# Optimization experiments

Hardware: AMD Instinct MI355X
Metric: run time of the kernel (lower is better)

Reference implementation:

```python
import jax, jax.numpy as jnp
import numpy as np

# --- fixed OpenCV filter kernels ---
# cv2.getGaussianKernel(3, 1): exp(-(i-1)^2/2), normalized -> [0.27407, 0.45186, 0.27407]
_g = np.exp(-((np.arange(3) - 1.0) ** 2) / 2.0)
GAUSS_1D = (_g / _g.sum()).astype(np.float32)
# cv2 Sobel/Laplacian ksize=9 separable parts (unnormalized, as cv2.Laplacian uses):
#   smoothing = binomial row C(8,k); second derivative = C(6,k) conv [1,-2,1]
SMOOTH_9 = np.array([1, 8, 28, 56, 70, 56, 28, 8, 1], dtype=np.float32)
D2_9 = np.array([1, 4, 4, -4, -10, -4, 4, 4, 1], dtype=np.float32)


def _depthwise_conv(x, k2d):
    """Depthwise 2D correlation with BORDER_REFLECT_101 padding (cv2 default).

    x: [N,H,W,C] float, k2d: [kh,kw] float (symmetric, so corr == conv)."""
    C = x.shape[-1]
    rh, rw = k2d.shape[0] // 2, k2d.shape[1] // 2
    # jnp 'reflect' == OpenCV BORDER_REFLECT_101 (edge pixel not duplicated)
    xp = jnp.pad(x, ((0, 0), (rh, rh), (rw, rw), (0, 0)), mode='reflect')
    k = jnp.broadcast_to(k2d[:, :, None, None], (k2d.shape[0], k2d.shape[1], 1, C))
    return jax.lax.conv_general_dilated(
        xp, k, window_strides=(1, 1), padding='VALID',
        dimension_numbers=('NHWC', 'HWIO', 'NHWC'),
        feature_group_count=C)


def setup_inputs() -> dict:
    key = jax.random.key(0)
    # uint8-range image batch, as the original layer feeds uint8 data to OpenCV
    x = jax.random.uniform(key, (32, 512, 512, 3), dtype=jnp.float32) * 255.0
    return {"x": x}


def reference(x) -> jnp.ndarray:
    g = jnp.asarray(GAUSS_1D)
    blur = _depthwise_conv(x, jnp.outer(g, g))  # GaussianBlur(ksize=3, sigma=1)
    lap_k = jnp.asarray(np.outer(SMOOTH_9, D2_9) + np.outer(D2_9, SMOOTH_9))
    lap = _depthwise_conv(blur, lap_k) + 1.0  # delta = 1
    # CV_8UC1 destination depth -> saturate to [0, 255]
    return jnp.clip(lap, 0.0, 255.0)
```

## Files before the change

### kernel.cpp

```cpp
#include <hip/hip_runtime.h>


#define TH 16
#define TW 32
#define FW (TW*3)
#define BF ((TW+8)*3)
#define BH (TH+8)
#define PH (TH+2)
#define VW 124
#define PW 108
#define HIMG 512
#define WIMG 512
#define ROWF (WIMG*3)

#define OFF_B 3120
#define SM_TOTAL 6000

__device__ __forceinline__ int reflect101(int i, int n) {
    i = (i < 0) ? -i : i;
    return (i >= n) ? (2 * n - 2 - i) : i;
}

__device__ __forceinline__ float c6dot(float f0, float f1, float f2, float f3,
                                       float f4, float f5, float f6) {
    return fmaf(20.f, f3, fmaf(6.f, f1 + f5, fmaf(15.f, f2 + f4, f0 + f6)));
}

__device__ __forceinline__ float4 c6dot4(const float4& a, const float4& b, const float4& c,
                                         const float4& d, const float4& e, const float4& f,
                                         const float4& g) {
    return make_float4(c6dot(a.x, b.x, c.x, d.x, e.x, f.x, g.x),
                       c6dot(a.y, b.y, c.y, d.y, e.y, f.y, g.y),
                       c6dot(a.z, b.z, c.z, d.z, e.z, f.z, g.z),
                       c6dot(a.w, b.w, c.w, d.w, e.w, f.w, g.w));
}

__device__ __forceinline__ float4 g3(const float4& a, const float4& b, const float4& c,
                                     float G0, float G1) {
    return make_float4(G0 * (a.x + c.x) + G1 * b.x,
                       G0 * (a.y + c.y) + G1 * b.y,
                       G0 * (a.z + c.z) + G1 * b.z,
                       G0 * (a.w + c.w) + G1 * b.w);
}

__global__ __launch_bounds__(256, 6)
void log_fused(const float* __restrict__ x, float* __restrict__ out) {
    __shared__ __align__(16) float smem[SM_TOTAL];
    float* const hblur = smem;
    float* const vq    = smem;
    float* const blur  = smem + OFF_B;
    float* const P     = smem + OFF_B;

    const int tid  = threadIdx.x;
    const int col0 = blockIdx.x * TW;
    const int row0 = blockIdx.y * TH;
    const int n    = blockIdx.z;

    const int R0    = max(0, row0 - 5);
    const int R1    = min(HIMG - 1, row0 + TH + 4);
    const int nrows = R1 - R0 + 1;

    const float G0 = 0.2740686190f, G1 = 0.4518627620f;

    const bool edgecol = (col0 == 0) || (col0 + TW == WIMG);
    if (!edgecol) {
        if (tid < 240) {
            const int cg = tid % 30;
            const int rg = tid / 30;
            const float* xb = x + ((size_t)n * HIMG + (size_t)(R0 + rg)) * ROWF
                                + (3 * (col0 - 4) + 4 * cg - 4);
            float* hb = hblur + rg * BF + 4 * cg;
            for (int r = rg; r < nrows; r += 8, xb += 8 * ROWF, hb += 8 * BF) {
                const float4 a = *(const float4*)(xb);
                const float4 b = *(const float4*)(xb + 4);
                const float4 c = *(const float4*)(xb + 8);
                float4 o;
                o.x = G0 * (a.y + b.w) + G1 * b.x;
                o.y = G0 * (a.z + c.x) + G1 * b.y;
                o.z = G0 * (a.w + c.y) + G1 * b.z;
                o.w = G0 * (b.x + c.z) + G1 * b.w;
                *(float4*)hb = o;
            }
        }
    } else {
        if (tid < 240) {
            const int lc  = tid % BF;
            const int rg  = tid / BF;
            const int lcp = lc / 3;
            const int ch  = lc - 3 * lcp;
            const int gc  = reflect101(col0 - 4 + lcp, WIMG);
            const int xm  = reflect101(gc - 1, WIMG) * 3 + ch;
            const int x0  = gc * 3 + ch;
            const int xp  = reflect101(gc + 1, WIMG) * 3 + ch;
            const float* xr = x + ((size_t)n * HIMG + (size_t)(R0 + rg)) * ROWF;
            for (int r = rg; r < nrows; r += 2, xr += 2 * ROWF) {
                hblur[r * BF + lc] = G0 * (xr[xm] + xr[xp]) + G1 * xr[x0];
            }
        }
    }
    __syncthreads();

    if (row0 > 0 && row0 + TH < HIMG) {
        for (int g = tid; g < 12 * 30; g += 256) {
            const int lp = g / 30;
            const int qc = g - lp * 30;
            const float* hb = hblur + (2 * lp) * BF + qc * 4;
            const float4 w0 = *(const float4*)(hb);
            const float4 w1 = *(const float4*)(hb + BF);
            const float4 w2 = *(const float4*)(hb + 2 * BF);
            const float4 w3 = *(const float4*)(hb + 3 * BF);
            float* bp = blur + (2 * lp) * BF + qc * 4;
            *(float4*)bp        = g3(w0, w1, w2, G0, G1);
            *(float4*)(bp + BF) = g3(w1, w2, w3, G0, G1);
        }
    } else {
        for (int g = tid; g < 12 * 30; g += 256) {
            const int lp = g / 30;
            const int qc = g - lp * 30;
            const int gg = row0 - 4 + 2 * lp;
            const int y0 = reflect101(gg, HIMG);
            const int y1 = reflect101(gg + 1, HIMG);
            const int lc = qc * 4;
            const float4 a0 = *(const float4*)&hblur[(reflect101(y0 - 1, HIMG) - R0) * BF + lc];
            const float4 a1 = *(const float4*)&hblur[(y0 - R0) * BF + lc];
            const float4 a2 = *(const float4*)&hblur[(reflect101(y0 + 1, HIMG) - R0) * BF + lc];
            const float4 b0 = *(const float4*)&hblur[(reflect101(y1 - 1, HIMG) - R0) * BF + lc];
            const float4 b1 = *(const float4*)&hblur[(y1 - R0) * BF + lc];
            const float4 b2 = *(const float4*)&hblur[(reflect101(y1 + 1, HIMG) - R0) * BF + lc];
            float* bp = blur + (2 * lp) * BF + lc;
            *(float4*)bp        = g3(a0, a1, a2, G0, G1);
            *(float4*)(bp + BF) = g3(b0, b1, b2, G0, G1);
        }
    }
    __syncthreads();

    for (int g = tid; g < 9 * 30; g += 256) {
        const int lp = g / 30;
        const int qc = g - lp * 30;
        const float* bp = blur + (2 * lp) * BF + qc * 4;
        float4 w[8];
        #pragma unroll
        for (int k = 0; k < 8; ++k)
            w[k] = *(const float4*)(bp + k * BF);
        float* vp = vq + (2 * lp) * VW + qc * 4;
        *(float4*)vp        = c6dot4(w[0], w[1], w[2], w[3], w[4], w[5], w[6]);
        *(float4*)(vp + VW) = c6dot4(w[1], w[2], w[3], w[4], w[5], w[6], w[7]);
    }
    __syncthreads();

    for (int g = tid; g < PH * 13; g += 256) {
        const int r  = g / 13;
        const int qp = g - r * 13;
        const float* v = vq + r * VW + qp * 8;
        float f[28];
        #pragma unroll
        for (int q = 0; q < 7; ++q) {
            const float4 w = *(const float4*)(v + 4 * q);
            f[4*q+0] = w.x; f[4*q+1] = w.y; f[4*q+2] = w.z; f[4*q+3] = w.w;
        }
        float p[8];
        #pragma unroll
        for (int j = 0; j < 8; ++j)
            p[j] = c6dot(f[j], f[j+3], f[j+6], f[j+9], f[j+12], f[j+15], f[j+18]);
        float* pr = P + r * PW + qp * 8;
        *(float4*)pr       = make_float4(p[0], p[1], p[2], p[3]);
        *(float4*)(pr + 4) = make_float4(p[4], p[5], p[6], p[7]);
    }
    __syncthreads();

    float* const outn = out + (size_t)n * HIMG * ROWF;
    for (int g = tid; g < TH * 12; g += 256) {
        const int i  = g / 12;
        const int qp = g - i * 12;
        const int o  = qp * 8;
        const float* pt = P + i * PW + o;
        const float* pm = pt + PW;
        const float* pb = pm + PW;
        float t[16], m[16], b[16];
        #pragma unroll
        for (int q = 0; q < 4; ++q) {
            const float4 vt = *(const float4*)(pt + 4 * q);
            t[4*q+0] = vt.x; t[4*q+1] = vt.y; t[4*q+2] = vt.z; t[4*q+3] = vt.w;
            const float4 vm = *(const float4*)(pm + 4 * q);
            m[4*q+0] = vm.x; m[4*q+1] = vm.y; m[4*q+2] = vm.z; m[4*q+3] = vm.w;
            const float4 vb = *(const float4*)(pb + 4 * q);
            b[4*q+0] = vb.x; b[4*q+1] = vb.y; b[4*q+2] = vb.z; b[4*q+3] = vb.w;
        }
        float o8[8];
        #pragma unroll
        for (int j = 0; j < 8; ++j) {
            const float c = m[j + 3];
            const float s = (t[j] - c) + (t[j + 6] - c) + (b[j] - c) + (b[j + 6] - c);
            const float v = fmaf(2.f, s, 1.f);
            o8[j] = fminf(fmaxf(v, 0.f), 255.f);
        }
        float* op = outn + (size_t)(row0 + i) * ROWF + (size_t)(col0 * 3 + o);
        *(float4*)op       = make_float4(o8[0], o8[1], o8[2], o8[3]);
        *(float4*)(op + 4) = make_float4(o8[4], o8[5], o8[6], o8[7]);
    }
}

extern "C" void kernel_launch(void* const* d_in, const int* in_sizes, int n_in,
                              void* d_out, int out_size, void* d_ws, size_t ws_size,
                              hipStream_t stream) {
    const float* x = (const float*)d_in[0];
    float* outp = (float*)d_out;
    const int nimg = in_sizes[0] / (HIMG * WIMG * 3);
    dim3 grid(WIMG / TW, HIMG / TH, nimg);
    log_fused<<<grid, dim3(256, 1, 1), 0, stream>>>(x, outp);
}
```

Before: 223.1 us.

## Fold Gaussian blur into binomial filter taps for interior tiles

For interior tiles, the 3-tap Gaussian is folded into the 7-tap binomial smoothing by convolving them analytically into a 9-tap kernel (U0..U4). Vertical and horizontal passes then read global memory directly and skip the separate blur stages and two barriers. Edge tiles now compute the 2D blur straight from global memory with reflect indexing in one pass, which lets shared memory shrink so launch bounds can rise to 8 blocks per SM. The cost is more global loads per thread (ten rows of float4) and different rounding from the folded coefficients.

New measurement: 327.0 us. +46.5%, slower.

```diff
diff --git a/kernel.cpp b/kernel.cpp
--- a/kernel.cpp
+++ b/kernel.cpp
@@ -3,22 +3,27 @@
 
 #define TH 16
 #define TW 32
-#define FW (TW*3)
-#define BF ((TW+8)*3)
-#define BH (TH+8)
-#define PH (TH+2)
-#define VW 124
-#define PW 108
 #define HIMG 512
 #define WIMG 512
 #define ROWF (WIMG*3)
 
-#define OFF_B 3120
-#define SM_TOTAL 6000
+#define VUW 132
+#define PW  108
+#define BLW 120
+#define VQW 124
+
+#define OFF_P  2376
+#define OFF_BL 2232
+#define SM_TOTAL 5112
 
 __device__ __forceinline__ int reflect101(int i, int n) {
     i = (i < 0) ? -i : i;
     return (i >= n) ? (2 * n - 2 - i) : i;
+}
+
+__device__ __forceinline__ float4 fma4(float s, const float4& a, const float4& b) {
+    return make_float4(fmaf(s, a.x, b.x), fmaf(s, a.y, b.y),
+                       fmaf(s, a.z, b.z), fmaf(s, a.w, b.w));
 }
 
 __device__ __forceinline__ float c6dot(float f0, float f1, float f2, float f3,
@@ -43,130 +48,165 @@
                        G0 * (a.w + c.w) + G1 * b.w);
 }
 
-__global__ __launch_bounds__(256, 6)
+#define U0 0.27406862f
+#define U1 2.09627447f
+#define U2 7.09627447f
+#define U3 13.90372553f
+#define U4 17.25931382f
+
+__global__ __launch_bounds__(256, 8)
 void log_fused(const float* __restrict__ x, float* __restrict__ out) {
     __shared__ __align__(16) float smem[SM_TOTAL];
-    float* const hblur = smem;
-    float* const vq    = smem;
-    float* const blur  = smem + OFF_B;
-    float* const P     = smem + OFF_B;
+    float* const vU   = smem;
+    float* const vq   = smem;
+    float* const blur = smem + OFF_BL;
+    float* const P    = smem + OFF_P;
 
     const int tid  = threadIdx.x;
     const int col0 = blockIdx.x * TW;
     const int row0 = blockIdx.y * TH;
     const int n    = blockIdx.z;
-
-    const int R0    = max(0, row0 - 5);
-    const int R1    = min(HIMG - 1, row0 + TH + 4);
-    const int nrows = R1 - R0 + 1;
+    const float* const xi = x + (size_t)n * HIMG * ROWF;
 
     const float G0 = 0.2740686190f, G1 = 0.4518627620f;
 
-    const bool edgecol = (col0 == 0) || (col0 + TW == WIMG);
-    if (!edgecol) {
-        if (tid < 240) {
-            const int cg = tid % 30;
-            const int rg = tid / 30;
-            const float* xb = x + ((size_t)n * HIMG + (size_t)(R0 + rg)) * ROWF
-                                + (3 * (col0 - 4) + 4 * cg - 4);
-            float* hb = hblur + rg * BF + 4 * cg;
-            for (int r = rg; r < nrows; r += 8, xb += 8 * ROWF, hb += 8 * BF) {
-                const float4 a = *(const float4*)(xb);
-                const float4 b = *(const float4*)(xb + 4);
-                const float4 c = *(const float4*)(xb + 8);
-                float4 o;
-                o.x = G0 * (a.y + b.w) + G1 * b.x;
-                o.y = G0 * (a.z + c.x) + G1 * b.y;
-                o.z = G0 * (a.w + c.y) + G1 * b.z;
-                o.w = G0 * (b.x + c.z) + G1 * b.w;
-                *(float4*)hb = o;
-            }
-        }
+    const bool interior = (row0 != 0) && (row0 != HIMG - TH) &&
+                          (col0 != 0) && (col0 != WIMG - TW);
+
+    if (interior) {
+        const float Uk[10] = {U0, U1, U2, U3, U4, U3, U2, U1, U0, 0.f};
+        for (int g = tid; g < 288; g += 256) {
+            const int q  = g & 31;
+            const int rp = g >> 5;
+            const float* xp = xi + (size_t)(row0 - 5 + 2 * rp) * ROWF
+                                 + (3 * col0 - 16 + 4 * q);
+            float4 a0 = make_float4(0.f, 0.f, 0.f, 0.f), a1 = a0;
+            #pragma unroll
+            for (int j = 0; j < 10; ++j) {
+                const float4 w = *(const float4*)(xp + (size_t)j * ROWF);
+                if (j < 9) a0 = fma4(Uk[j], w, a0);
+                if (j > 0) a1 = fma4(Uk[j - 1], w, a1);
+            }
+            float* vp = vU + (2 * rp) * VUW + 4 * q;
+            *(float4*)vp         = a0;
+            *(float4*)(vp + VUW) = a1;
+        }
+        __syncthreads();
+
+        if (tid < 234) {
+            const int t = tid % 13;
+            const int v = tid / 13;
+            const float* vr = vU + v * VUW + 8 * t;
+            float f[36];
+            #pragma unroll
+            for (int c = 0; c < 9; ++c) {
+                const float4 w = *(const float4*)(vr + 4 * c);
+                f[4*c+0] = w.x; f[4*c+1] = w.y; f[4*c+2] = w.z; f[4*c+3] = w.w;
+            }
+            float p[8];
+            #pragma unroll
+            for (int j = 0; j < 8; ++j) {
+                const float t0 = f[j + 1]  + f[j + 25];
+                const float t1 = f[j + 4]  + f[j + 22];
+                const float t2 = f[j + 7]  + f[j + 19];
+                const float t3 = f[j + 10] + f[j + 16];
+                p[j] = fmaf(U0, t0, fmaf(U1, t1, fmaf(U2, t2,
+                           fmaf(U3, t3, U4 * f[j + 13]))));
+            }
+            float* pr = P + v * PW + 8 * t;
+            *(float4*)pr       = make_float4(p[0], p[1], p[2], p[3]);
+            *(float4*)(pr + 4) = make_float4(p[4], p[5], p[6], p[7]);
+        }
+        __syncthreads();
     } else {
-        if (tid < 240) {
-            const int lc  = tid % BF;
-            const int rg  = tid / BF;
-            const int lcp = lc / 3;
-            const int ch  = lc - 3 * lcp;
-            const int gc  = reflect101(col0 - 4 + lcp, WIMG);
-            const int xm  = reflect101(gc - 1, WIMG) * 3 + ch;
-            const int x0  = gc * 3 + ch;
-            const int xp  = reflect101(gc + 1, WIMG) * 3 + ch;
-            const float* xr = x + ((size_t)n * HIMG + (size_t)(R0 + rg)) * ROWF;
-            for (int r = rg; r < nrows; r += 2, xr += 2 * ROWF) {
-                hblur[r * BF + lc] = G0 * (xr[xm] + xr[xp]) + G1 * xr[x0];
-            }
-        }
-    }
-    __syncthreads();
-
-    if (row0 > 0 && row0 + TH < HIMG) {
-        for (int g = tid; g < 12 * 30; g += 256) {
+        for (int e = tid; e < 720; e += 256) {
+            const int br = e / 30;
+            const int qc = e - br * 30;
+            const int gg = row0 - 4 + br;
+            const int gr = reflect101(gg, HIMG);
+            const int ym = reflect101(gr - 1, HIMG);
+            const int yp = reflect101(gr + 1, HIMG);
+            const int lcpmin = (4 * qc) / 3;
+            const int lcpmax = (4 * qc + 3) / 3;
+            const bool safe = (col0 - 5 + lcpmin >= 0) && (col0 - 3 + lcpmax <= WIMG - 1);
+            float4 r;
+            if (safe) {
+                const int fb = 3 * col0 - 16 + 4 * qc;
+                const float* r0 = xi + (size_t)ym * ROWF + fb;
+                const float* r1 = xi + (size_t)gr * ROWF + fb;
+                const float* r2 = xi + (size_t)yp * ROWF + fb;
+                float4 h[3];
+                #pragma unroll
+                for (int rr = 0; rr < 3; ++rr) {
+                    const float* rp = (rr == 0) ? r0 : (rr == 1) ? r1 : r2;
+                    const float4 a = *(const float4*)(rp);
+                    const float4 b = *(const float4*)(rp + 4);
+                    const float4 c = *(const float4*)(rp + 8);
+                    h[rr] = make_float4(G0 * (a.y + b.w) + G1 * b.x,
+                                        G0 * (a.z + c.x) + G1 * b.y,
+                                        G0 * (a.w + c.y) + G1 * b.z,
+                                        G0 * (b.x + c.z) + G1 * b.w);
+                }
+                r = g3(h[0], h[1], h[2], G0, G1);
+            } else {
+                float o[4];
+                #pragma unroll
+                for (int m = 0; m < 4; ++m) {
+                    const int lc  = 4 * qc + m;
+                    const int lcp = lc / 3;
+                    const int ch  = lc - 3 * lcp;
+                    const int gc  = reflect101(col0 - 4 + lcp, WIMG);
+                    const int xm  = reflect101(gc - 1, WIMG) * 3 + ch;
+                    const int x0  = gc * 3 + ch;
+                    const int xp2 = reflect101(gc + 1, WIMG) * 3 + ch;
+                    const float* r0 = xi + (size_t)ym * ROWF;
+                    const float* r1 = xi + (size_t)gr * ROWF;
+                    const float* r2 = xi + (size_t)yp * ROWF;
+                    const float h0 = G0 * (r0[xm] + r0[xp2]) + G1 * r0[x0];
+                    const float h1 = G0 * (r1[xm] + r1[xp2]) + G1 * r1[x0];
+                    const float h2 = G0 * (r2[xm] + r2[xp2]) + G1 * r2[x0];
+                    o[m] = G0 * (h0 + h2) + G1 * h1;
+                }
+                r = make_float4(o[0], o[1], o[2], o[3]);
+            }
+            *(float4*)&blur[br * BLW + 4 * qc] = r;
+        }
+        __syncthreads();
+
+        for (int g = tid; g < 270; g += 256) {
             const int lp = g / 30;
             const int qc = g - lp * 30;
-            const float* hb = hblur + (2 * lp) * BF + qc * 4;
-            const float4 w0 = *(const float4*)(hb);
-            const float4 w1 = *(const float4*)(hb + BF);
-            const float4 w2 = *(const float4*)(hb + 2 * BF);
-            const float4 w3 = *(const float4*)(hb + 3 * BF);
-            float* bp = blur + (2 * lp) * BF + qc * 4;
-            *(float4*)bp        = g3(w0, w1, w2, G0, G1);
-            *(float4*)(bp + BF) = g3(w1, w2, w3, G0, G1);
-        }
-    } else {
-        for (int g = tid; g < 12 * 30; g += 256) {
-            const int lp = g / 30;
-            const int qc = g - lp * 30;
-            const int gg = row0 - 4 + 2 * lp;
-            const int y0 = reflect101(gg, HIMG);
-            const int y1 = reflect101(gg + 1, HIMG);
-            const int lc = qc * 4;
-            const float4 a0 = *(const float4*)&hblur[(reflect101(y0 - 1, HIMG) - R0) * BF + lc];
-            const float4 a1 = *(const float4*)&hblur[(y0 - R0) * BF + lc];
-            const float4 a2 = *(const float4*)&hblur[(reflect101(y0 + 1, HIMG) - R0) * BF + lc];
-            const float4 b0 = *(const float4*)&hblur[(reflect101(y1 - 1, HIMG) - R0) * BF + lc];
-            const float4 b1 = *(const float4*)&hblur[(y1 - R0) * BF + lc];
-            const float4 b2 = *(const float4*)&hblur[(reflect101(y1 + 1, HIMG) - R0) * BF + lc];
-            float* bp = blur + (2 * lp) * BF + lc;
-            *(float4*)bp        = g3(a0, a1, a2, G0, G1);
-            *(float4*)(bp + BF) = g3(b0, b1, b2, G0, G1);
-        }
+            const float* bp = blur + (2 * lp) * BLW + 4 * qc;
+            float4 w[8];
+            #pragma unroll
+            for (int k = 0; k < 8; ++k)
+                w[k] = *(const float4*)(bp + k * BLW);
+            float* vp = vq + (2 * lp) * VQW + 4 * qc;
+            *(float4*)vp         = c6dot4(w[0], w[1], w[2], w[3], w[4], w[5], w[6]);
+            *(float4*)(vp + VQW) = c6dot4(w[1], w[2], w[3], w[4], w[5], w[6], w[7]);
+        }
+        __syncthreads();
+
+        if (tid < 234) {
+            const int t = tid % 13;
+            const int r = tid / 13;
+            const float* v = vq + r * VQW + 8 * t;
+            float f[28];
+            #pragma unroll
+            for (int c = 0; c < 7; ++c) {
+                const float4 w = *(const float4*)(v + 4 * c);
+                f[4*c+0] = w.x; f[4*c+1] = w.y; f[4*c+2] = w.z; f[4*c+3] = w.w;
+            }
+            float p[8];
+            #pragma unroll
+            for (int j = 0; j < 8; ++j)
+                p[j] = c6dot(f[j], f[j+3], f[j+6], f[j+9], f[j+12], f[j+15], f[j+18]);
+            float* pr = P + r * PW + 8 * t;
+            *(float4*)pr       = make_float4(p[0], p[1], p[2], p[3]);
+            *(float4*)(pr + 4) = make_float4(p[4], p[5], p[6], p[7]);
+        }
+        __syncthreads();
     }
-    __syncthreads();
-
-    for (int g = tid; g < 9 * 30; g += 256) {
-        const int lp = g / 30;
-        const int qc = g - lp * 30;
-        const float* bp = blur + (2 * lp) * BF + qc * 4;
-        float4 w[8];
-        #pragma unroll
-        for (int k = 0; k < 8; ++k)
-            w[k] = *(const float4*)(bp + k * BF);
-        float* vp = vq + (2 * lp) * VW + qc * 4;
-        *(float4*)vp        = c6dot4(w[0], w[1], w[2], w[3], w[4], w[5], w[6]);
-        *(float4*)(vp + VW) = c6dot4(w[1], w[2], w[3], w[4], w[5], w[6], w[7]);
-    }
-    __syncthreads();
-
-    for (int g = tid; g < PH * 13; g += 256) {
-        const int r  = g / 13;
-        const int qp = g - r * 13;
-        const float* v = vq + r * VW + qp * 8;
-        float f[28];
-        #pragma unroll
-        for (int q = 0; q < 7; ++q) {
-            const float4 w = *(const float4*)(v + 4 * q);
-            f[4*q+0] = w.x; f[4*q+1] = w.y; f[4*q+2] = w.z; f[4*q+3] = w.w;
-        }
-        float p[8];
-        #pragma unroll
-        for (int j = 0; j < 8; ++j)
-            p[j] = c6dot(f[j], f[j+3], f[j+6], f[j+9], f[j+12], f[j+15], f[j+18]);
-        float* pr = P + r * PW + qp * 8;
-        *(float4*)pr       = make_float4(p[0], p[1], p[2], p[3]);
-        *(float4*)(pr + 4) = make_float4(p[4], p[5], p[6], p[7]);
-    }
-    __syncthreads();
 
     float* const outn = out + (size_t)n * HIMG * ROWF;
     for (int g = tid; g < TH * 12; g += 256) {
```

## Fold vertical Gaussian into 7-tap binomial as single 9-tap vertical pass

Applied to the files above, without the earlier changes.

Composes the vertical 3-tap Gaussian with the vertical 7-tap binomial into one 9-tap vertical filter applied directly from the horizontally blurred tile. This removes one shared-memory stage and one barrier, and shrinks shared memory by re-laying out the buffers. Edge tiles use a reflect-aware path that recomputes the blur per tap. It also trims the unused middle-row loads in the final stage and swaps strided loops for guarded single passes. The interior path leaves 76 of 256 threads idle during the vertical pass.

Result: no change. 221.7 us (-0.7%).

```diff
diff --git a/kernel.cpp b/kernel.cpp
--- a/kernel.cpp
+++ b/kernel.cpp
@@ -3,9 +3,7 @@
 
 #define TH 16
 #define TW 32
-#define FW (TW*3)
 #define BF ((TW+8)*3)
-#define BH (TH+8)
 #define PH (TH+2)
 #define VW 124
 #define PW 108
@@ -13,26 +11,22 @@
 #define WIMG 512
 #define ROWF (WIMG*3)
 
-#define OFF_B 3120
-#define SM_TOTAL 6000
+#define OFF_VQ 3120
+#define SM_TOTAL 5352
 
 __device__ __forceinline__ int reflect101(int i, int n) {
     i = (i < 0) ? -i : i;
     return (i >= n) ? (2 * n - 2 - i) : i;
 }
 
+__device__ __forceinline__ float4 fma4(float s, const float4& a, const float4& b) {
+    return make_float4(fmaf(s, a.x, b.x), fmaf(s, a.y, b.y),
+                       fmaf(s, a.z, b.z), fmaf(s, a.w, b.w));
+}
+
 __device__ __forceinline__ float c6dot(float f0, float f1, float f2, float f3,
                                        float f4, float f5, float f6) {
     return fmaf(20.f, f3, fmaf(6.f, f1 + f5, fmaf(15.f, f2 + f4, f0 + f6)));
-}
-
-__device__ __forceinline__ float4 c6dot4(const float4& a, const float4& b, const float4& c,
-                                         const float4& d, const float4& e, const float4& f,
-                                         const float4& g) {
-    return make_float4(c6dot(a.x, b.x, c.x, d.x, e.x, f.x, g.x),
-                       c6dot(a.y, b.y, c.y, d.y, e.y, f.y, g.y),
-                       c6dot(a.z, b.z, c.z, d.z, e.z, f.z, g.z),
-                       c6dot(a.w, b.w, c.w, d.w, e.w, f.w, g.w));
 }
 
 __device__ __forceinline__ float4 g3(const float4& a, const float4& b, const float4& c,
@@ -43,13 +37,18 @@
                        G0 * (a.w + c.w) + G1 * b.w);
 }
 
+#define U0 0.27406862f
+#define U1 2.09627447f
+#define U2 7.09627447f
+#define U3 13.90372553f
+#define U4 17.25931382f
+
 __global__ __launch_bounds__(256, 6)
 void log_fused(const float* __restrict__ x, float* __restrict__ out) {
     __shared__ __align__(16) float smem[SM_TOTAL];
     float* const hblur = smem;
-    float* const vq    = smem;
-    float* const blur  = smem + OFF_B;
-    float* const P     = smem + OFF_B;
+    float* const P     = smem;
+    float* const vq    = smem + OFF_VQ;
 
     const int tid  = threadIdx.x;
     const int col0 = blockIdx.x * TW;
@@ -61,6 +60,9 @@
     const int nrows = R1 - R0 + 1;
 
     const float G0 = 0.2740686190f, G1 = 0.4518627620f;
+
+    if (tid < PH)
+        *(float4*)&vq[tid * VW + 120] = make_float4(0.f, 0.f, 0.f, 0.f);
 
     const bool edgecol = (col0 == 0) || (col0 + TW == WIMG);
     if (!edgecol) {
@@ -100,91 +102,87 @@
     }
     __syncthreads();
 
-    if (row0 > 0 && row0 + TH < HIMG) {
-        for (int g = tid; g < 12 * 30; g += 256) {
-            const int lp = g / 30;
-            const int qc = g - lp * 30;
-            const float* hb = hblur + (2 * lp) * BF + qc * 4;
-            const float4 w0 = *(const float4*)(hb);
-            const float4 w1 = *(const float4*)(hb + BF);
-            const float4 w2 = *(const float4*)(hb + 2 * BF);
-            const float4 w3 = *(const float4*)(hb + 3 * BF);
-            float* bp = blur + (2 * lp) * BF + qc * 4;
-            *(float4*)bp        = g3(w0, w1, w2, G0, G1);
-            *(float4*)(bp + BF) = g3(w1, w2, w3, G0, G1);
+    if (row0 != 0 && row0 != HIMG - TH) {
+        if (tid < 180) {
+            const int rg = tid / 30;
+            const int qc = tid % 30;
+            const float U9k[9] = {U0, U1, U2, U3, U4, U3, U2, U1, U0};
+            const float* hb = hblur + (3 * rg) * BF + 4 * qc;
+            float4 a0 = make_float4(0.f, 0.f, 0.f, 0.f), a1 = a0, a2 = a0;
+            #pragma unroll
+            for (int j = 0; j < 11; ++j) {
+                const float4 w = *(const float4*)(hb + j * BF);
+                if (j <= 8)           a0 = fma4(U9k[j],     w, a0);
+                if (j >= 1 && j <= 9) a1 = fma4(U9k[j - 1], w, a1);
+                if (j >= 2)           a2 = fma4(U9k[j - 2], w, a2);
+            }
+            float* vp = vq + (3 * rg) * VW + 4 * qc;
+            *(float4*)vp            = a0;
+            *(float4*)(vp + VW)     = a1;
+            *(float4*)(vp + 2 * VW) = a2;
         }
     } else {
-        for (int g = tid; g < 12 * 30; g += 256) {
-            const int lp = g / 30;
-            const int qc = g - lp * 30;
-            const int gg = row0 - 4 + 2 * lp;
-            const int y0 = reflect101(gg, HIMG);
-            const int y1 = reflect101(gg + 1, HIMG);
-            const int lc = qc * 4;
-            const float4 a0 = *(const float4*)&hblur[(reflect101(y0 - 1, HIMG) - R0) * BF + lc];
-            const float4 a1 = *(const float4*)&hblur[(y0 - R0) * BF + lc];
-            const float4 a2 = *(const float4*)&hblur[(reflect101(y0 + 1, HIMG) - R0) * BF + lc];
-            const float4 b0 = *(const float4*)&hblur[(reflect101(y1 - 1, HIMG) - R0) * BF + lc];
-            const float4 b1 = *(const float4*)&hblur[(y1 - R0) * BF + lc];
-            const float4 b2 = *(const float4*)&hblur[(reflect101(y1 + 1, HIMG) - R0) * BF + lc];
-            float* bp = blur + (2 * lp) * BF + lc;
-            *(float4*)bp        = g3(a0, a1, a2, G0, G1);
-            *(float4*)(bp + BF) = g3(b0, b1, b2, G0, G1);
+        const float C6k[7] = {1.f, 6.f, 15.f, 20.f, 15.f, 6.f, 1.f};
+        for (int g = tid; g < PH * 30; g += 256) {
+            const int r  = g / 30;
+            const int qc = g - r * 30;
+            const int gb = row0 - 4 + r;
+            float4 acc = make_float4(0.f, 0.f, 0.f, 0.f);
+            #pragma unroll
+            for (int k = 0; k < 7; ++k) {
+                const int y  = reflect101(gb + k, HIMG);
+                const int ym = reflect101(y - 1, HIMG) - R0;
+                const int yp = reflect101(y + 1, HIMG) - R0;
+                const float4 a = *(const float4*)&hblur[ym * BF + 4 * qc];
+                const float4 b = *(const float4*)&hblur[(y - R0) * BF + 4 * qc];
+                const float4 c = *(const float4*)&hblur[yp * BF + 4 * qc];
+                acc = fma4(C6k[k], g3(a, b, c, G0, G1), acc);
+            }
+            *(float4*)&vq[r * VW + 4 * qc] = acc;
         }
     }
     __syncthreads();
 
-    for (int g = tid; g < 9 * 30; g += 256) {
-        const int lp = g / 30;
-        const int qc = g - lp * 30;
-        const float* bp = blur + (2 * lp) * BF + qc * 4;
-        float4 w[8];
-        #pragma unroll
-        for (int k = 0; k < 8; ++k)
-            w[k] = *(const float4*)(bp + k * BF);
-        float* vp = vq + (2 * lp) * VW + qc * 4;
-        *(float4*)vp        = c6dot4(w[0], w[1], w[2], w[3], w[4], w[5], w[6]);
-        *(float4*)(vp + VW) = c6dot4(w[1], w[2], w[3], w[4], w[5], w[6], w[7]);
-    }
-    __syncthreads();
-
-    for (int g = tid; g < PH * 13; g += 256) {
-        const int r  = g / 13;
-        const int qp = g - r * 13;
-        const float* v = vq + r * VW + qp * 8;
+    if (tid < PH * 13) {
+        const int qp = tid % 13;
+        const int r  = tid / 13;
+        const float* v = vq + r * VW + 8 * qp;
         float f[28];
         #pragma unroll
-        for (int q = 0; q < 7; ++q) {
-            const float4 w = *(const float4*)(v + 4 * q);
-            f[4*q+0] = w.x; f[4*q+1] = w.y; f[4*q+2] = w.z; f[4*q+3] = w.w;
+        for (int c = 0; c < 7; ++c) {
+            const float4 w = *(const float4*)(v + 4 * c);
+            f[4*c+0] = w.x; f[4*c+1] = w.y; f[4*c+2] = w.z; f[4*c+3] = w.w;
         }
         float p[8];
         #pragma unroll
         for (int j = 0; j < 8; ++j)
             p[j] = c6dot(f[j], f[j+3], f[j+6], f[j+9], f[j+12], f[j+15], f[j+18]);
-        float* pr = P + r * PW + qp * 8;
+        float* pr = P + r * PW + 8 * qp;
         *(float4*)pr       = make_float4(p[0], p[1], p[2], p[3]);
         *(float4*)(pr + 4) = make_float4(p[4], p[5], p[6], p[7]);
     }
     __syncthreads();
 
     float* const outn = out + (size_t)n * HIMG * ROWF;
-    for (int g = tid; g < TH * 12; g += 256) {
-        const int i  = g / 12;
-        const int qp = g - i * 12;
+    if (tid < TH * 12) {
+        const int qp = tid % 12;
+        const int i  = tid / 12;
         const int o  = qp * 8;
         const float* pt = P + i * PW + o;
         const float* pm = pt + PW;
         const float* pb = pm + PW;
-        float t[16], m[16], b[16];
+        float t[16], m[12], b[16];
         #pragma unroll
         for (int q = 0; q < 4; ++q) {
             const float4 vt = *(const float4*)(pt + 4 * q);
             t[4*q+0] = vt.x; t[4*q+1] = vt.y; t[4*q+2] = vt.z; t[4*q+3] = vt.w;
+            const float4 vb = *(const float4*)(pb + 4 * q);
+            b[4*q+0] = vb.x; b[4*q+1] = vb.y; b[4*q+2] = vb.z; b[4*q+3] = vb.w;
+        }
+        #pragma unroll
+        for (int q = 0; q < 3; ++q) {
             const float4 vm = *(const float4*)(pm + 4 * q);
             m[4*q+0] = vm.x; m[4*q+1] = vm.y; m[4*q+2] = vm.z; m[4*q+3] = vm.w;
-            const float4 vb = *(const float4*)(pb + 4 * q);
-            b[4*q+0] = vb.x; b[4*q+1] = vb.y; b[4*q+2] = vb.z; b[4*q+3] = vb.w;
         }
         float o8[8];
         #pragma unroll
```
